# Kernel tuning notes

Hardware: AMD Instinct MI355X
Metric: run time of the kernel (lower is better)

Reference implementation:

```python
import jax, jax.numpy as jnp
import numpy as np

B, T, C = 1, 2048, 1024
H, KVH = 16, 4
D = C // H            # 64
KV = KVH * D          # 256
EPS = 1e-6
SCALE = 1.0 / np.sqrt(D)
ROPE_BASE = 10000.0


def setup_inputs() -> dict:
    key = jax.random.key(0)
    ks = jax.random.split(key, 8)
    s = 0.02
    return dict(
        x=jax.random.normal(ks[0], (B, T, C), jnp.float32),
        Wq=jax.random.normal(ks[1], (C, C), jnp.float32) * s,
        Wk=jax.random.normal(ks[2], (KV, C), jnp.float32) * s,
        Wv=jax.random.normal(ks[3], (KV, C), jnp.float32) * s,
        Wo=jax.random.normal(ks[4], (C, C), jnp.float32) * s,
        q_norm_w=jnp.ones((C,), jnp.float32),
        k_norm_w=jnp.ones((KV,), jnp.float32),
        fgate_w=jax.random.normal(ks[5], (H, C), jnp.float32) * s,
        fgate_b=jnp.zeros((H,), jnp.float32),
        weight_lambda=jax.random.normal(ks[6], (C, H), jnp.float32) * s,
    )


def _rmsnorm(x, w):
    var = jnp.mean(x * x, axis=-1, keepdims=True)
    return x * jax.lax.rsqrt(var + EPS) * w


def _rotate_half(x):
    x1, x2 = jnp.split(x, 2, axis=-1)
    return jnp.concatenate([-x2, x1], axis=-1)


def _apply_rope(q, k):
    # q: [B,H,T,D], k: [B,KVH,T,D]; position_ids = arange(T)
    inv_freq = 1.0 / (ROPE_BASE ** (jnp.arange(0, D, 2, dtype=jnp.float32) / D))
    freqs = jnp.outer(jnp.arange(T, dtype=jnp.float32), inv_freq)  # [T, D/2]
    emb = jnp.concatenate([freqs, freqs], axis=-1)                 # [T, D]
    cos = jnp.cos(emb)[None, None]                                  # [1,1,T,D]
    sin = jnp.sin(emb)[None, None]
    return q * cos + _rotate_half(q) * sin, k * cos + _rotate_half(k) * sin


def _forward(x, Wq, Wk, Wv, Wo, q_norm_w, k_norm_w, fgate_w, fgate_b, weight_lambda):
    q = _rmsnorm(x @ Wq.T, q_norm_w)          # [B,T,C]
    k = _rmsnorm(x @ Wk.T, k_norm_w)          # [B,T,KV]
    v = x @ Wv.T                              # [B,T,KV]
    q = q.reshape(B, T, H, D).transpose(0, 2, 1, 3)     # [B,H,T,D]
    k = k.reshape(B, T, KVH, D).transpose(0, 2, 1, 3)   # [B,KVH,T,D]
    v = v.reshape(B, T, KVH, D).transpose(0, 2, 1, 3)
    q, k = _apply_rope(q, k)
    # GQA: repeat_interleave kv heads
    g = H // KVH
    k = jnp.repeat(k, g, axis=1)              # [B,H,T,D]
    v = jnp.repeat(v, g, axis=1)
    # Forgetting gate (FoX): log f_t per head, with elu-based lambda scaling
    lam = jax.nn.elu(x @ weight_lambda) + 1.0            # [B,T,H]
    logit = (x @ fgate_w.T + fgate_b) * lam              # [B,T,H]
    log_f = (jax.nn.log_sigmoid(logit) / (lam + 1e-3)).transpose(0, 2, 1)  # [B,H,T]
    c = jnp.cumsum(log_f, axis=-1)                       # [B,H,T]
    bias = c[..., :, None] - c[..., None, :]             # [B,H,T,T]: sum_{t=j+1..i} log f_t
    scores = jnp.einsum('bhid,bhjd->bhij', q, k) * SCALE + bias
    causal = jnp.tril(jnp.ones((T, T), dtype=bool))
    scores = jnp.where(causal, scores, -jnp.inf)
    p = jax.nn.softmax(scores, axis=-1)
    y = jnp.einsum('bhij,bhjd->bhid', p, v)              # [B,H,T,D]
    y = y.transpose(0, 2, 1, 3).reshape(B, T, C)
    return y @ Wo.T


def reference(x, Wq, Wk, Wv, Wo, q_norm_w, k_norm_w, fgate_w, fgate_b, weight_lambda):
    return _forward(x, Wq, Wk, Wv, Wo, q_norm_w, k_norm_w, fgate_w, fgate_b, weight_lambda)
```

## Files before the change

### kernel.cpp

```cpp
#include <hip/hip_runtime.h>

typedef __bf16 bf16x8 __attribute__((ext_vector_type(8)));
typedef float f32x4 __attribute__((ext_vector_type(4)));

#define MFMA_BF16 __builtin_amdgcn_mfma_f32_16x16x32_bf16

static constexpr int T_ = 2048;
static constexpr int C_ = 1024;
static constexpr int H_ = 16;
static constexpr int KVH_ = 4;
static constexpr int D_ = 64;
static constexpr float SCALE_ = 0.125f;
static constexpr float MSHIFT_ = 10.0f;

__device__ inline void cvt8(__bf16* dst, const float* src) {
  float4 a = *(const float4*)src;
  float4 b = *(const float4*)(src + 4);
  bf16x8 r;
  r[0] = (__bf16)a.x; r[1] = (__bf16)a.y; r[2] = (__bf16)a.z; r[3] = (__bf16)a.w;
  r[4] = (__bf16)b.x; r[5] = (__bf16)b.y; r[6] = (__bf16)b.z; r[7] = (__bf16)b.w;
  *(bf16x8*)dst = r;
}

__global__ __launch_bounds__(256) void cvt_kernel(
    const float* __restrict__ x,  const float* __restrict__ wq,
    const float* __restrict__ wk, const float* __restrict__ wv,
    const float* __restrict__ wo, const float* __restrict__ wl,
    __bf16* __restrict__ xb,  __bf16* __restrict__ wqb,
    __bf16* __restrict__ wkb, __bf16* __restrict__ wvb,
    __bf16* __restrict__ wob, float* __restrict__ wlT)
{
  size_t i8 = ((size_t)blockIdx.x * 256 + threadIdx.x) * 8;
  if (i8 < 2097152)       cvt8(xb  + i8,            x  + i8);
  else if (i8 < 3145728)  cvt8(wqb + (i8-2097152),  wq + (i8-2097152));
  else if (i8 < 3407872)  cvt8(wkb + (i8-3145728),  wk + (i8-3145728));
  else if (i8 < 3670016)  cvt8(wvb + (i8-3407872),  wv + (i8-3407872));
  else if (i8 < 4718592)  cvt8(wob + (i8-3670016),  wo + (i8-3670016));
  else {
    size_t r = i8 - 4718592;
    if (r < 16384) {
#pragma unroll
      for (int j = 0; j < 8; ++j) {
        size_t idx = r + j;
        size_t hh = idx >> 10, c = idx & 1023;
        wlT[idx] = wl[c * 16 + hh];
      }
    }
  }
}

__global__ __launch_bounds__(256) void gates_kernel(
    const float* __restrict__ x, const float* __restrict__ fw,
    const float* __restrict__ fb, const float* __restrict__ wlT,
    float* __restrict__ logf)
{
  const int t = blockIdx.x;
  const int tid = threadIdx.x, w = tid >> 6, lane = tid & 63;
  float xv[16];
#pragma unroll
  for (int i = 0; i < 16; ++i)
    xv[i] = x[(size_t)t * C_ + i * 64 + lane];
#pragma unroll
  for (int u = 0; u < 4; ++u) {
    int h = w * 4 + u;
    float s1 = 0.f, s2 = 0.f;
#pragma unroll
    for (int i = 0; i < 16; ++i) {
      int cidx = i * 64 + lane;
      s1 += xv[i] * wlT[(size_t)h * C_ + cidx];
      s2 += xv[i] * fw[(size_t)h * C_ + cidx];
    }
    for (int m = 32; m; m >>= 1) {
      s1 += __shfl_xor(s1, m);
      s2 += __shfl_xor(s2, m);
    }
    if (lane == 0) {
      float lam = (s1 > 0.f ? s1 : expm1f(s1)) + 1.0f;
      float logit = (s2 + fb[h]) * lam;
      float ls = (logit >= 0.f) ? -log1pf(expf(-logit))
                                : (logit - log1pf(expf(logit)));
      logf[(size_t)h * T_ + t] = ls / (lam + 1e-3f);
    }
  }
}

template <int BM>
__global__ __launch_bounds__(256) void gemm_bt_kernel(
    const __bf16* __restrict__ A, int K, int N,
    const __bf16* __restrict__ B0, int e0,
    const __bf16* __restrict__ B1, int e1,
    const __bf16* __restrict__ B2,
    float* __restrict__ outF)
{
  __shared__ __bf16 la[BM * 40];
  __shared__ __bf16 lb[128 * 40];
  const int m0 = blockIdx.y * BM;
  const int n0 = blockIdx.x * 128;
  const __bf16* Bs; int nrel;
  if (n0 < e0)      { Bs = B0; nrel = n0; }
  else if (n0 < e1) { Bs = B1; nrel = n0 - e0; }
  else              { Bs = B2; nrel = n0 - e1; }
  const int tid = threadIdx.x;
  const int arow = tid >> 2, acol = (tid & 3) * 8;
  const __bf16* ap = A  + (size_t)(m0   + arow) * K + acol;
  const __bf16* bp = Bs + (size_t)(nrel + arow) * K + acol;
  const int w = tid >> 6, lane = tid & 63, lq = lane >> 4, ln = lane & 15;
  const int wm = (w >> 1) * (BM / 2), wn = (w & 1) * 64;
  constexpr int FM = BM / 32;
  f32x4 acc[FM][4] = {};
  for (int k0 = 0; k0 < K; k0 += 32) {
    bf16x8 a0 = *(const bf16x8*)(ap + k0);
    bf16x8 a1{};
    if (BM == 128) a1 = *(const bf16x8*)(ap + (size_t)64 * K + k0);
    bf16x8 b0 = *(const bf16x8*)(bp + k0);
    bf16x8 b1 = *(const bf16x8*)(bp + (size_t)64 * K + k0);
    __syncthreads();
    *(bf16x8*)(la + arow * 40 + acol) = a0;
    if (BM == 128) *(bf16x8*)(la + (arow + 64) * 40 + acol) = a1;
    *(bf16x8*)(lb + arow * 40 + acol) = b0;
    *(bf16x8*)(lb + (arow + 64) * 40 + acol) = b1;
    __syncthreads();
    bf16x8 af[FM], bfr[4];
#pragma unroll
    for (int i = 0; i < FM; ++i)
      af[i] = *(const bf16x8*)(la + (wm + i * 16 + ln) * 40 + lq * 8);
#pragma unroll
    for (int j = 0; j < 4; ++j)
      bfr[j] = *(const bf16x8*)(lb + (wn + j * 16 + ln) * 40 + lq * 8);
#pragma unroll
    for (int i = 0; i < FM; ++i)
#pragma unroll
      for (int j = 0; j < 4; ++j)
        acc[i][j] = MFMA_BF16(af[i], bfr[j], acc[i][j], 0, 0, 0);
  }
#pragma unroll
  for (int i = 0; i < FM; ++i)
#pragma unroll
    for (int j = 0; j < 4; ++j)
#pragma unroll
      for (int r = 0; r < 4; ++r) {
        int row = m0 + wm + i * 16 + lq * 4 + r;
        int col = n0 + wn + j * 16 + ln;
        outF[(size_t)row * N + col] = acc[i][j][r];
      }
}

__global__ __launch_bounds__(64) void cumsum_kernel(
    const float* __restrict__ logf, float* __restrict__ csum)
{
  const int h = blockIdx.x;
  const int lane = threadIdx.x;
  float carry = 0.f;
  for (int ch = 0; ch < T_ / 64; ++ch) {
    float v = logf[(size_t)h * T_ + ch * 64 + lane];
#pragma unroll
    for (int d = 1; d < 64; d <<= 1) {
      float tv = __shfl_up(v, d);
      if (lane >= d) v += tv;
    }
    v += carry;
    csum[(size_t)h * T_ + ch * 64 + lane] = v;
    carry = __shfl(v, 63);
  }
}

__global__ __launch_bounds__(256) void normrope_kernel(
    const float* __restrict__ qkv, const float* __restrict__ qw,
    const float* __restrict__ kw, __bf16* __restrict__ qh,
    __bf16* __restrict__ kh, __bf16* __restrict__ vh)
{
  const int t = blockIdx.x, tid = threadIdx.x;
  __shared__ float qn[1024];
  __shared__ float kn[256];
  __shared__ float red[16];
  __shared__ float rc[32], rs[32];
  if (tid < 32) {
    float fr = (float)t * exp2f((float)tid * -0.41524101186404527f);
    float sn, cs;
    sincosf(fr, &sn, &cs);
    rc[tid] = cs; rs[tid] = sn;
  }
  const float* row = qkv + (size_t)t * 1536;
  float4 q4 = *(const float4*)(row + tid * 4);
  float kvl = row[1024 + tid];
  float vvl = row[1280 + tid];
  float ssq = q4.x * q4.x + q4.y * q4.y + q4.z * q4.z + q4.w * q4.w;
  float ssk = kvl * kvl;
  const int lane = tid & 63, w = tid >> 6;
  for (int m = 32; m; m >>= 1) {
    ssq += __shfl_xor(ssq, m);
    ssk += __shfl_xor(ssk, m);
  }
  if (lane == 0) { red[w] = ssq; red[8 + w] = ssk; }
  __syncthreads();
  float sq = red[0] + red[1] + red[2] + red[3];
  float sk = red[8] + red[9] + red[10] + red[11];
  float rq = rsqrtf(sq * (1.0f / 1024.f) + 1e-6f);
  float rk = rsqrtf(sk * (1.0f / 256.f) + 1e-6f);
  qn[tid * 4 + 0] = q4.x * rq * qw[tid * 4 + 0];
  qn[tid * 4 + 1] = q4.y * rq * qw[tid * 4 + 1];
  qn[tid * 4 + 2] = q4.z * rq * qw[tid * 4 + 2];
  qn[tid * 4 + 3] = q4.w * rq * qw[tid * 4 + 3];
  kn[tid] = kvl * rk * kw[tid];
  __syncthreads();
#pragma unroll
  for (int u = 0; u < 4; ++u) {
    int cidx = tid * 4 + u;
    int hh = cidx >> 6, d = cidx & 63, i = d & 31;
    float cs = rc[i], sn = rs[i];
    float val = (d < 32) ? (qn[cidx] * cs - qn[cidx + 32] * sn)
                         : (qn[cidx] * cs + qn[cidx - 32] * sn);
    qh[(size_t)hh * T_ * D_ + (size_t)t * D_ + d] = (__bf16)val;
  }
  {
    int d = tid & 63, kvhh = tid >> 6, i = d & 31;
    float cs = rc[i], sn = rs[i];
    float kval = (d < 32) ? (kn[tid] * cs - kn[tid + 32] * sn)
                          : (kn[tid] * cs + kn[tid - 32] * sn);
    kh[(size_t)kvhh * T_ * D_ + (size_t)t * D_ + d] = (__bf16)kval;
    vh[(size_t)kvhh * T_ * D_ + (size_t)t * D_ + d] = (__bf16)vvl;
  }
}

__global__ __launch_bounds__(256) void vtrans_kernel(
    const __bf16* __restrict__ vh, __bf16* __restrict__ vt)
{
  const int tb = blockIdx.x, kvh = blockIdx.y;
  __shared__ __bf16 tile[64][72];
  const int tid = threadIdx.x;
  const int r = tid >> 2, cb = (tid & 3) * 16;
  const __bf16* src = vh + (size_t)kvh * T_ * D_ + (size_t)(tb * 64 + r) * D_ + cb;
  bf16x8 v0 = *(const bf16x8*)(src);
  bf16x8 v1 = *(const bf16x8*)(src + 8);
  *(bf16x8*)(&tile[r][cb]) = v0;
  *(bf16x8*)(&tile[r][cb + 8]) = v1;
  __syncthreads();
  bf16x8 o0, o1;
#pragma unroll
  for (int j = 0; j < 8; ++j) o0[j] = tile[cb + j][r];
#pragma unroll
  for (int j = 0; j < 8; ++j) o1[j] = tile[cb + 8 + j][r];
  __bf16* dst = vt + (size_t)kvh * D_ * T_ + (size_t)r * T_ + tb * 64 + cb;
  *(bf16x8*)(dst) = o0;
  *(bf16x8*)(dst + 8) = o1;
}

__global__ __launch_bounds__(256) void attn_part_kernel(
    const __bf16* __restrict__ qh, const __bf16* __restrict__ kh,
    const __bf16* __restrict__ vt, const float* __restrict__ csum,
    float* __restrict__ po, float* __restrict__ pls)
{
  const int ib = blockIdx.x, h = blockIdx.y, z = blockIdx.z;
  const int jbeg = z * 8;
  if (jbeg > ib) return;
  const int jend = min(jbeg + 8, ib + 1);
  const int i0 = ib * 64, kvh = h >> 2;
  __shared__ __bf16 kt[64 * 72];
  __shared__ __bf16 vtt[64 * 72];
  __shared__ __bf16 pt[4][16 * 72];
  const int tid = threadIdx.x;
  const int w = tid >> 6, lane = tid & 63, lq = lane >> 4, ln = lane & 15;
  const int srow = tid >> 2, scol = (tid & 3) * 16;
  const __bf16* kbase = kh + (size_t)kvh * T_ * D_;
  const __bf16* vbase = vt + (size_t)kvh * D_ * T_;
  const __bf16* qp = qh + ((size_t)h * T_ + i0 + w * 16 + ln) * D_;
  bf16x8 aq0 = *(const bf16x8*)(qp + lq * 8);
  bf16x8 aq1 = *(const bf16x8*)(qp + 32 + lq * 8);
  float ci[4];
#pragma unroll
  for (int r = 0; r < 4; ++r)
    ci[r] = csum[(size_t)h * T_ + i0 + w * 16 + lq * 4 + r];
  f32x4 o[4] = {};
  f32x4 ls = {0.f, 0.f, 0.f, 0.f};
  bf16x8 ones;
#pragma unroll
  for (int j = 0; j < 8; ++j) ones[j] = (__bf16)1.0f;
  __bf16* pw = &pt[w][0];

  bf16x8 kr0 = *(const bf16x8*)(kbase + (size_t)(jbeg * 64 + srow) * D_ + scol);
  bf16x8 kr1 = *(const bf16x8*)(kbase + (size_t)(jbeg * 64 + srow) * D_ + scol + 8);
  bf16x8 vr0 = *(const bf16x8*)(vbase + (size_t)srow * T_ + jbeg * 64 + scol);
  bf16x8 vr1 = *(const bf16x8*)(vbase + (size_t)srow * T_ + jbeg * 64 + scol + 8);
  *(bf16x8*)(kt + srow * 72 + scol) = kr0;
  *(bf16x8*)(kt + srow * 72 + scol + 8) = kr1;
  *(bf16x8*)(vtt + srow * 72 + scol) = vr0;
  *(bf16x8*)(vtt + srow * 72 + scol + 8) = vr1;
  __syncthreads();

  auto tilebody = [&](int j0, bool diag) {
    f32x4 s[4];
    const f32x4 zf = {0.f, 0.f, 0.f, 0.f};
#pragma unroll
    for (int jj = 0; jj < 4; ++jj) {
      bf16x8 bk0 = *(const bf16x8*)(kt + (jj * 16 + ln) * 72 + lq * 8);
      bf16x8 bk1 = *(const bf16x8*)(kt + (jj * 16 + ln) * 72 + 32 + lq * 8);
      s[jj] = MFMA_BF16(aq0, bk0, zf, 0, 0, 0);
      s[jj] = MFMA_BF16(aq1, bk1, s[jj], 0, 0, 0);
    }
    float cj[4];
#pragma unroll
    for (int jj = 0; jj < 4; ++jj)
      cj[jj] = csum[(size_t)h * T_ + j0 + jj * 16 + ln];
#pragma unroll
    for (int jj = 0; jj < 4; ++jj)
#pragma unroll
      for (int r = 0; r < 4; ++r) {
        float arg = fmaf(s[jj][r], SCALE_, ci[r] - cj[jj] - MSHIFT_);
        float p = __expf(arg);
        if (diag && (jj * 16 + ln > w * 16 + lq * 4 + r)) p = 0.f;
        pw[(lq * 4 + r) * 72 + jj * 16 + ln] = (__bf16)p;
      }
    asm volatile("s_waitcnt lgkmcnt(0)" ::: "memory");
    bf16x8 pa0 = *(const bf16x8*)(pw + ln * 72 + lq * 8);
    bf16x8 pa1 = *(const bf16x8*)(pw + ln * 72 + 32 + lq * 8);
    ls = MFMA_BF16(pa0, ones, ls, 0, 0, 0);
    ls = MFMA_BF16(pa1, ones, ls, 0, 0, 0);
#pragma unroll
    for (int dd = 0; dd < 4; ++dd) {
      bf16x8 bv0 = *(const bf16x8*)(vtt + (dd * 16 + ln) * 72 + lq * 8);
      bf16x8 bv1 = *(const bf16x8*)(vtt + (dd * 16 + ln) * 72 + 32 + lq * 8);
      o[dd] = MFMA_BF16(pa0, bv0, o[dd], 0, 0, 0);
      o[dd] = MFMA_BF16(pa1, bv1, o[dd], 0, 0, 0);
    }
  };

  for (int jt = jbeg; jt < jend - 1; ++jt) {
    const int j0n = (jt + 1) * 64;
    kr0 = *(const bf16x8*)(kbase + (size_t)(j0n + srow) * D_ + scol);
    kr1 = *(const bf16x8*)(kbase + (size_t)(j0n + srow) * D_ + scol + 8);
    vr0 = *(const bf16x8*)(vbase + (size_t)srow * T_ + j0n + scol);
    vr1 = *(const bf16x8*)(vbase + (size_t)srow * T_ + j0n + scol + 8);
    tilebody(jt * 64, false);
    __syncthreads();
    *(bf16x8*)(kt + srow * 72 + scol) = kr0;
    *(bf16x8*)(kt + srow * 72 + scol + 8) = kr1;
    *(bf16x8*)(vtt + srow * 72 + scol) = vr0;
    *(bf16x8*)(vtt + srow * 72 + scol + 8) = vr1;
    __syncthreads();
  }
  tilebody((jend - 1) * 64, (jend - 1) == ib);

  const size_t pbase = ((size_t)(h * 32 + ib) * 4 + z) * 4096;
  const size_t lbase = ((size_t)(h * 32 + ib) * 4 + z) * 64;
#pragma unroll
  for (int dd = 0; dd < 4; ++dd)
#pragma unroll
    for (int r = 0; r < 4; ++r) {
      int row = w * 16 + lq * 4 + r;
      int col = dd * 16 + ln;
      po[pbase + row * 64 + col] = o[dd][r];
    }
  if (ln == 0)
#pragma unroll
    for (int r = 0; r < 4; ++r)
      pls[lbase + w * 16 + lq * 4 + r] = ls[r];
}

__global__ __launch_bounds__(256) void attn_red_kernel(
    const float* __restrict__ po, const float* __restrict__ pls,
    __bf16* __restrict__ y)
{
  const int ib = blockIdx.x, h = blockIdx.y;
  const int nch = ib / 8 + 1;
  const int tid = threadIdx.x;
  __shared__ float lss[64];
  const size_t pbase = (size_t)(h * 32 + ib) * 4 * 4096;
  const size_t lbase = (size_t)(h * 32 + ib) * 4 * 64;
  if (tid < 64) {
    float s = 0.f;
    for (int c = 0; c < nch; ++c) s += pls[lbase + c * 64 + tid];
    lss[tid] = s;
  }
  __syncthreads();
#pragma unroll 4
  for (int u = 0; u < 16; ++u) {
    int idx = u * 256 + tid;
    int row = idx >> 6, col = idx & 63;
    float acc = 0.f;
    for (int c = 0; c < nch; ++c) acc += po[pbase + c * 4096 + idx];
    y[(size_t)(ib * 64 + row) * C_ + h * 64 + col] = (__bf16)(acc / lss[row]);
  }
}

extern "C" void kernel_launch(void* const* d_in, const int* in_sizes, int n_in,
                              void* d_out, int out_size, void* d_ws, size_t ws_size,
                              hipStream_t stream) {
  const float* x   = (const float*)d_in[0];
  const float* Wq  = (const float*)d_in[1];
  const float* Wk  = (const float*)d_in[2];
  const float* Wv  = (const float*)d_in[3];
  const float* Wo  = (const float*)d_in[4];
  const float* qnw = (const float*)d_in[5];
  const float* knw = (const float*)d_in[6];
  const float* fgw = (const float*)d_in[7];
  const float* fgb = (const float*)d_in[8];
  const float* wl  = (const float*)d_in[9];

  char* ws = (char*)d_ws;
  size_t off = 0;
  float*  qkv  = (float*)(ws + off);  off += (size_t)T_ * 1536 * 4;
  __bf16* xb   = (__bf16*)(ws + off); off += (size_t)T_ * C_ * 2;
  __bf16* wqb  = (__bf16*)(ws + off); off += (size_t)C_ * C_ * 2;
  __bf16* wkb  = (__bf16*)(ws + off); off += (size_t)256 * C_ * 2;
  __bf16* wvb  = (__bf16*)(ws + off); off += (size_t)256 * C_ * 2;
  float*  po   = (float*)ws;
  off = (size_t)16 * 32 * 4 * 4096 * 4;
  float*  logf = (float*)(ws + off);  off += (size_t)H_ * T_ * 4;
  float*  csum = (float*)(ws + off);  off += (size_t)H_ * T_ * 4;
  __bf16* qh   = (__bf16*)(ws + off); off += (size_t)H_ * T_ * D_ * 2;
  __bf16* kh   = (__bf16*)(ws + off); off += (size_t)KVH_ * T_ * D_ * 2;
  __bf16* vh   = (__bf16*)(ws + off); off += (size_t)KVH_ * T_ * D_ * 2;
  __bf16* vt   = (__bf16*)(ws + off); off += (size_t)KVH_ * T_ * D_ * 2;
  __bf16* y    = (__bf16*)(ws + off); off += (size_t)T_ * C_ * 2;
  __bf16* wob  = (__bf16*)(ws + off); off += (size_t)C_ * C_ * 2;
  float*  pls  = (float*)(ws + off);  off += (size_t)16 * 32 * 4 * 64 * 4;
  float*  wlT  = (float*)(ws + off);  off += (size_t)H_ * C_ * 4;

  cvt_kernel<<<2312, 256, 0, stream>>>(x, Wq, Wk, Wv, Wo, wl,
                                       xb, wqb, wkb, wvb, wob, wlT);
  gemm_bt_kernel<64><<<dim3(12, 32), 256, 0, stream>>>(
      xb, 1024, 1536, wqb, 1024, wkb, 1280, wvb, qkv);
  gates_kernel<<<T_, 256, 0, stream>>>(x, fgw, fgb, wlT, logf);
  cumsum_kernel<<<H_, 64, 0, stream>>>(logf, csum);
  normrope_kernel<<<T_, 256, 0, stream>>>(qkv, qnw, knw, qh, kh, vh);
  vtrans_kernel<<<dim3(T_ / 64, KVH_), 256, 0, stream>>>(vh, vt);
  attn_part_kernel<<<dim3(32, 16, 4), 256, 0, stream>>>(qh, kh, vt, csum, po, pls);
  attn_red_kernel<<<dim3(32, 16), 256, 0, stream>>>(po, pls, y);
  gemm_bt_kernel<64><<<dim3(8, 32), 256, 0, stream>>>(
      y, 1024, 1024, wob, 1024, wob, 1024, wob, (float*)d_out);
}
```

Before: 219.2 us.

## Restructure attention partial kernel: 128-row query blocks, direct K/V register loads, transposed MFMA

Each block of the attention partial kernel now covers 128 query rows instead of 64, with each wave handling 32 rows so every K/V fragment feeds two query sub-tiles. K and V fragments are loaded straight from global memory into registers, replacing the shared-memory staging and block barriers. The MFMA operands are swapped so S^T is computed, which lets P be written to LDS as packed bf16x4. Row sums are accumulated in scalar registers with shuffle reductions instead of an extra MFMA against ones. Launch bounds request 3 blocks per SM. The risk is redundant global K/V traffic across waves, relying on L1/L2, plus higher register pressure.

```diff
diff --git a/kernel.cpp b/kernel.cpp
--- a/kernel.cpp
+++ b/kernel.cpp
@@ -1,6 +1,7 @@
 #include <hip/hip_runtime.h>
 
 typedef __bf16 bf16x8 __attribute__((ext_vector_type(8)));
+typedef __bf16 bf16x4 __attribute__((ext_vector_type(4)));
 typedef float f32x4 __attribute__((ext_vector_type(4)));
 
 #define MFMA_BF16 __builtin_amdgcn_mfma_f32_16x16x32_bf16
@@ -245,115 +246,108 @@
   *(bf16x8*)(dst + 8) = o1;
 }
 
-__global__ __launch_bounds__(256) void attn_part_kernel(
+__global__ __launch_bounds__(256, 3) void attn_part_kernel(
     const __bf16* __restrict__ qh, const __bf16* __restrict__ kh,
     const __bf16* __restrict__ vt, const float* __restrict__ csum,
     float* __restrict__ po, float* __restrict__ pls)
 {
-  const int ib = blockIdx.x, h = blockIdx.y, z = blockIdx.z;
+  const int qs = blockIdx.x, h = blockIdx.y, z = blockIdx.z;
+  const int jt_lim = 2 * qs + 2;
   const int jbeg = z * 8;
-  if (jbeg > ib) return;
-  const int jend = min(jbeg + 8, ib + 1);
-  const int i0 = ib * 64, kvh = h >> 2;
-  __shared__ __bf16 kt[64 * 72];
-  __shared__ __bf16 vtt[64 * 72];
-  __shared__ __bf16 pt[4][16 * 72];
+  if (jbeg >= jt_lim) return;
+  const int jend = min(jbeg + 8, jt_lim);
+  const int kvh = h >> 2;
   const int tid = threadIdx.x;
   const int w = tid >> 6, lane = tid & 63, lq = lane >> 4, ln = lane & 15;
-  const int srow = tid >> 2, scol = (tid & 3) * 16;
+  const int ibase = qs * 128 + w * 32;
+  __shared__ __bf16 pts[8][16 * 72];
+  __bf16* p0 = &pts[w * 2 + 0][0];
+  __bf16* p1 = &pts[w * 2 + 1][0];
+
   const __bf16* kbase = kh + (size_t)kvh * T_ * D_;
   const __bf16* vbase = vt + (size_t)kvh * D_ * T_;
-  const __bf16* qp = qh + ((size_t)h * T_ + i0 + w * 16 + ln) * D_;
-  bf16x8 aq0 = *(const bf16x8*)(qp + lq * 8);
-  bf16x8 aq1 = *(const bf16x8*)(qp + 32 + lq * 8);
-  float ci[4];
-#pragma unroll
-  for (int r = 0; r < 4; ++r)
-    ci[r] = csum[(size_t)h * T_ + i0 + w * 16 + lq * 4 + r];
-  f32x4 o[4] = {};
-  f32x4 ls = {0.f, 0.f, 0.f, 0.f};
-  bf16x8 ones;
-#pragma unroll
-  for (int j = 0; j < 8; ++j) ones[j] = (__bf16)1.0f;
-  __bf16* pw = &pt[w][0];
-
-  bf16x8 kr0 = *(const bf16x8*)(kbase + (size_t)(jbeg * 64 + srow) * D_ + scol);
-  bf16x8 kr1 = *(const bf16x8*)(kbase + (size_t)(jbeg * 64 + srow) * D_ + scol + 8);
-  bf16x8 vr0 = *(const bf16x8*)(vbase + (size_t)srow * T_ + jbeg * 64 + scol);
-  bf16x8 vr1 = *(const bf16x8*)(vbase + (size_t)srow * T_ + jbeg * 64 + scol + 8);
-  *(bf16x8*)(kt + srow * 72 + scol) = kr0;
-  *(bf16x8*)(kt + srow * 72 + scol + 8) = kr1;
-  *(bf16x8*)(vtt + srow * 72 + scol) = vr0;
-  *(bf16x8*)(vtt + srow * 72 + scol + 8) = vr1;
-  __syncthreads();
-
-  auto tilebody = [&](int j0, bool diag) {
-    f32x4 s[4];
-    const f32x4 zf = {0.f, 0.f, 0.f, 0.f};
+  const float*  cb    = csum + (size_t)h * T_;
+
+  const __bf16* qp0 = qh + ((size_t)h * T_ + ibase + ln) * D_;
+  const __bf16* qp1 = qh + ((size_t)h * T_ + ibase + 16 + ln) * D_;
+  bf16x8 q00 = *(const bf16x8*)(qp0 + lq * 8);
+  bf16x8 q01 = *(const bf16x8*)(qp0 + 32 + lq * 8);
+  bf16x8 q10 = *(const bf16x8*)(qp1 + lq * 8);
+  bf16x8 q11 = *(const bf16x8*)(qp1 + 32 + lq * 8);
+  const float bci0 = cb[ibase + ln] - MSHIFT_;
+  const float bci1 = cb[ibase + 16 + ln] - MSHIFT_;
+
+  f32x4 o0[4] = {}, o1[4] = {};
+  float ls0 = 0.f, ls1 = 0.f;
+  const f32x4 zf = {0.f, 0.f, 0.f, 0.f};
+
+  for (int jt = jbeg; jt < jend; ++jt) {
+    const int j0 = jt * 64;
+    if (j0 > ibase + 31) continue;
+    const bool edge = (j0 + 63 > ibase);
+    f32x4 s0[4], s1[4];
 #pragma unroll
     for (int jj = 0; jj < 4; ++jj) {
-      bf16x8 bk0 = *(const bf16x8*)(kt + (jj * 16 + ln) * 72 + lq * 8);
-      bf16x8 bk1 = *(const bf16x8*)(kt + (jj * 16 + ln) * 72 + 32 + lq * 8);
-      s[jj] = MFMA_BF16(aq0, bk0, zf, 0, 0, 0);
-      s[jj] = MFMA_BF16(aq1, bk1, s[jj], 0, 0, 0);
-    }
-    float cj[4];
-#pragma unroll
-    for (int jj = 0; jj < 4; ++jj)
-      cj[jj] = csum[(size_t)h * T_ + j0 + jj * 16 + ln];
-#pragma unroll
-    for (int jj = 0; jj < 4; ++jj)
+      const __bf16* kp = kbase + (size_t)(j0 + jj * 16 + ln) * D_;
+      bf16x8 k0 = *(const bf16x8*)(kp + lq * 8);
+      bf16x8 k1 = *(const bf16x8*)(kp + 32 + lq * 8);
+      s0[jj] = MFMA_BF16(k0, q00, zf, 0, 0, 0);
+      s0[jj] = MFMA_BF16(k1, q01, s0[jj], 0, 0, 0);
+      s1[jj] = MFMA_BF16(k0, q10, zf, 0, 0, 0);
+      s1[jj] = MFMA_BF16(k1, q11, s1[jj], 0, 0, 0);
+    }
+#pragma unroll
+    for (int jj = 0; jj < 4; ++jj) {
+      f32x4 cj = *(const f32x4*)(cb + j0 + jj * 16 + lq * 4);
+      bf16x4 pv0, pv1;
 #pragma unroll
       for (int r = 0; r < 4; ++r) {
-        float arg = fmaf(s[jj][r], SCALE_, ci[r] - cj[jj] - MSHIFT_);
-        float p = __expf(arg);
-        if (diag && (jj * 16 + ln > w * 16 + lq * 4 + r)) p = 0.f;
-        pw[(lq * 4 + r) * 72 + jj * 16 + ln] = (__bf16)p;
+        int jabs = j0 + jj * 16 + lq * 4 + r;
+        float e0 = __expf(fmaf(s0[jj][r], SCALE_, bci0 - cj[r]));
+        float e1 = __expf(fmaf(s1[jj][r], SCALE_, bci1 - cj[r]));
+        if (edge) {
+          if (jabs > ibase + ln) e0 = 0.f;
+          if (jabs > ibase + 16 + ln) e1 = 0.f;
+        }
+        pv0[r] = (__bf16)e0; pv1[r] = (__bf16)e1;
+        ls0 += e0; ls1 += e1;
       }
+      *(bf16x4*)(p0 + ln * 72 + jj * 16 + lq * 4) = pv0;
+      *(bf16x4*)(p1 + ln * 72 + jj * 16 + lq * 4) = pv1;
+    }
     asm volatile("s_waitcnt lgkmcnt(0)" ::: "memory");
-    bf16x8 pa0 = *(const bf16x8*)(pw + ln * 72 + lq * 8);
-    bf16x8 pa1 = *(const bf16x8*)(pw + ln * 72 + 32 + lq * 8);
-    ls = MFMA_BF16(pa0, ones, ls, 0, 0, 0);
-    ls = MFMA_BF16(pa1, ones, ls, 0, 0, 0);
+    bf16x8 pa00 = *(const bf16x8*)(p0 + ln * 72 + lq * 8);
+    bf16x8 pa01 = *(const bf16x8*)(p0 + ln * 72 + 32 + lq * 8);
+    bf16x8 pa10 = *(const bf16x8*)(p1 + ln * 72 + lq * 8);
+    bf16x8 pa11 = *(const bf16x8*)(p1 + ln * 72 + 32 + lq * 8);
 #pragma unroll
     for (int dd = 0; dd < 4; ++dd) {
-      bf16x8 bv0 = *(const bf16x8*)(vtt + (dd * 16 + ln) * 72 + lq * 8);
-      bf16x8 bv1 = *(const bf16x8*)(vtt + (dd * 16 + ln) * 72 + 32 + lq * 8);
-      o[dd] = MFMA_BF16(pa0, bv0, o[dd], 0, 0, 0);
-      o[dd] = MFMA_BF16(pa1, bv1, o[dd], 0, 0, 0);
-    }
-  };
-
-  for (int jt = jbeg; jt < jend - 1; ++jt) {
-    const int j0n = (jt + 1) * 64;
-    kr0 = *(const bf16x8*)(kbase + (size_t)(j0n + srow) * D_ + scol);
-    kr1 = *(const bf16x8*)(kbase + (size_t)(j0n + srow) * D_ + scol + 8);
-    vr0 = *(const bf16x8*)(vbase + (size_t)srow * T_ + j0n + scol);
-    vr1 = *(const bf16x8*)(vbase + (size_t)srow * T_ + j0n + scol + 8);
-    tilebody(jt * 64, false);
-    __syncthreads();
-    *(bf16x8*)(kt + srow * 72 + scol) = kr0;
-    *(bf16x8*)(kt + srow * 72 + scol + 8) = kr1;
-    *(bf16x8*)(vtt + srow * 72 + scol) = vr0;
-    *(bf16x8*)(vtt + srow * 72 + scol + 8) = vr1;
-    __syncthreads();
-  }
-  tilebody((jend - 1) * 64, (jend - 1) == ib);
-
-  const size_t pbase = ((size_t)(h * 32 + ib) * 4 + z) * 4096;
-  const size_t lbase = ((size_t)(h * 32 + ib) * 4 + z) * 64;
-#pragma unroll
-  for (int dd = 0; dd < 4; ++dd)
-#pragma unroll
-    for (int r = 0; r < 4; ++r) {
-      int row = w * 16 + lq * 4 + r;
-      int col = dd * 16 + ln;
-      po[pbase + row * 64 + col] = o[dd][r];
-    }
-  if (ln == 0)
-#pragma unroll
-    for (int r = 0; r < 4; ++r)
-      pls[lbase + w * 16 + lq * 4 + r] = ls[r];
+      const __bf16* vp = vbase + (size_t)(dd * 16 + ln) * T_ + j0;
+      bf16x8 v0 = *(const bf16x8*)(vp + lq * 8);
+      bf16x8 v1 = *(const bf16x8*)(vp + 32 + lq * 8);
+      o0[dd] = MFMA_BF16(v0, pa00, o0[dd], 0, 0, 0);
+      o0[dd] = MFMA_BF16(v1, pa01, o0[dd], 0, 0, 0);
+      o1[dd] = MFMA_BF16(v0, pa10, o1[dd], 0, 0, 0);
+      o1[dd] = MFMA_BF16(v1, pa11, o1[dd], 0, 0, 0);
+    }
+  }
+  ls0 += __shfl_xor(ls0, 16); ls0 += __shfl_xor(ls0, 32);
+  ls1 += __shfl_xor(ls1, 16); ls1 += __shfl_xor(ls1, 32);
+
+  const int ib64 = qs * 2 + (w >> 1);
+  const size_t pbase = ((size_t)(h * 32 + ib64) * 4 + z) * 4096;
+  const size_t lbase = ((size_t)(h * 32 + ib64) * 4 + z) * 64;
+  const int lrow0 = (w & 1) * 32 + ln;
+  const int lrow1 = lrow0 + 16;
+#pragma unroll
+  for (int dd = 0; dd < 4; ++dd) {
+    *(f32x4*)(po + pbase + (size_t)lrow0 * 64 + dd * 16 + lq * 4) = o0[dd];
+    *(f32x4*)(po + pbase + (size_t)lrow1 * 64 + dd * 16 + lq * 4) = o1[dd];
+  }
+  if (lq == 0) {
+    pls[lbase + lrow0] = ls0;
+    pls[lbase + lrow1] = ls1;
+  }
 }
 
 __global__ __launch_bounds__(256) void attn_red_kernel(
@@ -424,7 +418,7 @@
   cumsum_kernel<<<H_, 64, 0, stream>>>(logf, csum);
   normrope_kernel<<<T_, 256, 0, stream>>>(qkv, qnw, knw, qh, kh, vh);
   vtrans_kernel<<<dim3(T_ / 64, KVH_), 256, 0, stream>>>(vh, vt);
-  attn_part_kernel<<<dim3(32, 16, 4), 256, 0, stream>>>(qh, kh, vt, csum, po, pls);
+  attn_part_kernel<<<dim3(16, 16, 4), 256, 0, stream>>>(qh, kh, vt, csum, po, pls);
   attn_red_kernel<<<dim3(32, 16), 256, 0, stream>>>(po, pls, y);
   gemm_bt_kernel<64><<<dim3(8, 32), 256, 0, stream>>>(
       y, 1024, 1024, wob, 1024, wob, 1024, wob, (float*)d_out);
```

After: 243.8 us. +11.2%, slower.
